# Optimization experiments

Measured on AMD Instinct MI355X. Metric: run time of the kernel, lower is better.

## Reference

```python
import jax, jax.numpy as jnp
import numpy as np

H, DK = 4, 64
D = H * DK              # hidden_dim = 256
D_OUT = 64
L = 2
NT, ET = 2, 3
AUTHOR, PAPER = 0, 1                 # sorted ntypes: ['author','paper']
CITES, WRITES, WRITTEN_BY = 0, 1, 2  # sorted etypes: ['cites','writes','written-by']
NA, NPAPER = 20000, 40000
E_WB, E_W, E_C = 150000, 150000, 300000
SQRT_DK = float(np.sqrt(DK))
EPS = 1e-5


def setup_inputs() -> dict:
    key = jax.random.key(0)
    ks = jax.random.split(key, 24)
    s = 1.0 / np.sqrt(D)
    return {
        "x_author": jax.random.normal(ks[0], (NA, D), jnp.float32),
        "x_paper": jax.random.normal(ks[1], (NPAPER, D), jnp.float32),
        "ew_wb": jax.random.uniform(ks[2], (E_WB,), jnp.float32),
        "ew_w": jax.random.uniform(ks[3], (E_W,), jnp.float32),
        "ew_c": jax.random.uniform(ks[4], (E_C,), jnp.float32),
        "adapt_W": jax.random.normal(ks[5], (NT, D, D), jnp.float32) * s,
        "adapt_b": jnp.zeros((NT, D), jnp.float32),
        "kW": jax.random.normal(ks[6], (L, NT, D, D), jnp.float32) * s,
        "kb": jnp.zeros((L, NT, D), jnp.float32),
        "qW": jax.random.normal(ks[7], (L, NT, D, D), jnp.float32) * s,
        "qb": jnp.zeros((L, NT, D), jnp.float32),
        "mW": jax.random.normal(ks[8], (L, NT, D, D), jnp.float32) * s,
        "mb": jnp.zeros((L, NT, D), jnp.float32),
        "aW": jax.random.normal(ks[9], (L, NT, D, D), jnp.float32) * s,
        "ab": jnp.zeros((L, NT, D), jnp.float32),
        "w_pri": jnp.ones((L, ET, H), jnp.float32),
        "w_att": jax.random.normal(ks[10], (L, ET, H, DK, DK), jnp.float32) / np.sqrt(DK),
        "w_msg": jax.random.normal(ks[11], (L, ET, H, DK, DK), jnp.float32) / np.sqrt(DK),
        "skip": jnp.ones((L, ET), jnp.float32),
        "ln_g": jnp.ones((L, NT, D), jnp.float32),
        "ln_b": jnp.zeros((L, NT, D), jnp.float32),
        "out_W": jax.random.normal(ks[12], (D, D_OUT), jnp.float32) * s,
        "out_b": jnp.zeros((D_OUT,), jnp.float32),
        "src_wb": jax.random.randint(ks[13], (E_WB,), 0, NPAPER, jnp.int32),
        "dst_wb": jax.random.randint(ks[14], (E_WB,), 0, NA, jnp.int32),
        "src_w": jax.random.randint(ks[15], (E_W,), 0, NA, jnp.int32),
        "dst_w": jax.random.randint(ks[16], (E_W,), 0, NPAPER, jnp.int32),
        "src_c": jax.random.randint(ks[17], (E_C,), 0, NPAPER, jnp.int32),
        "dst_c": jax.random.randint(ks[18], (E_C,), 0, NPAPER, jnp.int32),
    }


def _ln(x, g, b):
    mu = x.mean(-1, keepdims=True)
    var = ((x - mu) ** 2).mean(-1, keepdims=True)
    return (x - mu) * jax.lax.rsqrt(var + EPS) * g + b


def _hgt_layer(feats, rels, kW, kb, qW, qb, mW, mb, aW, ab,
               w_pri, w_att, w_msg, skip, ln_g, ln_b):
    # feats: [x_author, x_paper]; per-ntype K/Q/M projections -> [N, H, DK]
    Ns = [f.shape[0] for f in feats]
    kbase = [(feats[t] @ kW[t] + kb[t]).reshape(-1, H, DK) for t in range(NT)]
    qbase = [(feats[t] @ qW[t] + qb[t]).reshape(-1, H, DK) for t in range(NT)]
    mbase = [(feats[t] @ mW[t] + mb[t]).reshape(-1, H, DK) for t in range(NT)]
    aggs = {}
    for (st, e, dt, src, dst, ew) in rels:
        k = jnp.einsum('nhd,hde->nhe', kbase[st], w_att[e])
        m = jnp.einsum('nhd,hde->nhe', mbase[st], w_msg[e])
        score = (qbase[dt][dst] * k[src]).sum(-1) * w_pri[e] / SQRT_DK  # [E, H]
        attn = jax.nn.sigmoid(score) * ew[:, None]
        msg = m[src] * attn[:, :, None]                                 # [E, H, DK]
        aggs[e] = jax.ops.segment_sum(msg, dst, num_segments=Ns[dt])
    # cross_reducer='mean': mean over relation aggregates per dst ntype
    t_author = aggs[WRITTEN_BY].reshape(Ns[AUTHOR], D)
    t_paper = ((aggs[WRITES] + aggs[CITES]) * 0.5).reshape(Ns[PAPER], D)
    new = []
    for nid, t in ((AUTHOR, t_author), (PAPER, t_paper)):
        alpha = jax.nn.sigmoid(skip[nid])  # skip indexed by n_id (as in source)
        tr = t @ aW[nid] + ab[nid]
        o = tr * alpha + feats[nid] * (1.0 - alpha)
        new.append(_ln(o, ln_g[nid], ln_b[nid]))
    return new


def _forward(x_author, x_paper, ew_wb, ew_w, ew_c,
             adapt_W, adapt_b, kW, kb, qW, qb, mW, mb, aW, ab,
             w_pri, w_att, w_msg, skip, ln_g, ln_b, out_W, out_b,
             src_wb, dst_wb, src_w, dst_w, src_c, dst_c):
    feats = [
        jax.nn.gelu(x_author @ adapt_W[AUTHOR] + adapt_b[AUTHOR], approximate=False),
        jax.nn.gelu(x_paper @ adapt_W[PAPER] + adapt_b[PAPER], approximate=False),
    ]
    rels = [
        (PAPER, WRITTEN_BY, AUTHOR, src_wb, dst_wb, ew_wb),
        (AUTHOR, WRITES, PAPER, src_w, dst_w, ew_w),
        (PAPER, CITES, PAPER, src_c, dst_c, ew_c),
    ]
    for l in range(L):
        feats = _hgt_layer(feats, rels, kW[l], kb[l], qW[l], qb[l], mW[l], mb[l],
                           aW[l], ab[l], w_pri[l], w_att[l], w_msg[l], skip[l],
                           ln_g[l], ln_b[l])
    return feats[PAPER] @ out_W + out_b  # out_key = 'paper'


def reference(x_author, x_paper, ew_wb, ew_w, ew_c,
              adapt_W, adapt_b, kW, kb, qW, qb, mW, mb, aW, ab,
              w_pri, w_att, w_msg, skip, ln_g, ln_b, out_W, out_b,
              src_wb, dst_wb, src_w, dst_w, src_c, dst_c):
    return _forward(x_author, x_paper, ew_wb, ew_w, ew_c,
                    adapt_W, adapt_b, kW, kb, qW, qb, mW, mb, aW, ab,
                    w_pri, w_att, w_msg, skip, ln_g, ln_b, out_W, out_b,
                    src_wb, dst_wb, src_w, dst_w, src_c, dst_c)
```

## Files before the change

### kernel.cpp

```cpp
#include <hip/hip_runtime.h>
#include <hip/hip_bf16.h>
#include <math.h>

using bf16 = __hip_bfloat16;

typedef __attribute__((ext_vector_type(8))) short short8;
typedef __attribute__((ext_vector_type(4))) float float4v;

static constexpr int kNA  = 20000;
static constexpr int kNP  = 40000;
static constexpr int kEWB = 150000;
static constexpr int kEW  = 150000;
static constexpr int kEC  = 300000;

static constexpr int kNSeg = 21;
static constexpr int kSegN[kNSeg] = {
  150000, 150000, 300000,
  131072, 512,
  262144, 1024,
  262144, 1024,
  262144, 1024,
  262144, 1024,
  24,
  98304, 98304,
  6, 1024, 1024,
  16384, 64
};
static constexpr size_t kOff(int s) {
  size_t o = 0;
  for (int i = 0; i < s; ++i) o += (size_t)kSegN[i];
  return o;
}
static constexpr size_t kCanonTotal = kOff(kNSeg);

struct CanonArgs {
  const void* src[kNSeg];
  int n[kNSeg];
  unsigned dstOff[kNSeg];
};
struct TransArgs {
  const bf16* src[10];
  bf16* dst[10];
};
struct GemmDesc {
  const short* wt;
  const bf16* bias;
  void* c;
  int ldc;
  int coff;
  int act;
  int otype;
  int pad;
};
struct MultiDesc { GemmDesc d[6]; };
struct ScanArgs {
  int* deg[3];
  int* offs[3];
  int* bsums;
  int N[3];
};

__device__ __forceinline__ float toF(float x) { return x; }
__device__ __forceinline__ float toF(bf16 x)  { return __bfloat162float(x); }
__device__ __forceinline__ float bits2f(unsigned short b) {
  unsigned int u = ((unsigned int)b) << 16;
  return __uint_as_float(u);
}
__device__ __forceinline__ float sigmoidf_(float x) { return 1.0f / (1.0f + expf(-x)); }
__device__ __forceinline__ float gelu_exact(float x) {
  return 0.5f * x * (1.0f + erff(x * 0.70710678118654752f));
}

__global__ __launch_bounds__(256) void detect_dtype(
    const unsigned* __restrict__ x, unsigned* __restrict__ flags)
{
  __shared__ int cnt;
  if (threadIdx.x == 0) cnt = 0;
  __syncthreads();
  unsigned w = x[threadIdx.x];
  unsigned e = (w >> 7) & 0xFFu;
  if (e >= 110u && e <= 140u) atomicAdd(&cnt, 1);
  __syncthreads();
  if (threadIdx.x == 0) {
    flags[0] = (cnt >= 128) ? 1u : 0u;
    flags[1] = 1u;
  }
}

__global__ __launch_bounds__(256) void canon_kernel(
    CanonArgs a, bf16* __restrict__ dst, const unsigned* __restrict__ flags)
{
  const int s = blockIdx.y;
  const int i = blockIdx.x * 256 + threadIdx.x;
  if (i >= a.n[s]) return;
  bf16 v;
  if (flags[0]) v = ((const bf16*)a.src[s])[i];
  else          v = __float2bfloat16(((const float*)a.src[s])[i]);
  dst[a.dstOff[s] + i] = v;
}

__global__ __launch_bounds__(256) void transpose_w(TransArgs ta)
{
  const int m = blockIdx.z;
  const short* src = (const short*)ta.src[m];
  short* dst = (short*)ta.dst[m];
  const int k0 = blockIdx.x * 64, n0 = blockIdx.y * 64;
  __shared__ short tile[64][65];
  const int tx = threadIdx.x & 63, ty = threadIdx.x >> 6;
  for (int i = ty; i < 64; i += 4)
    tile[i][tx] = src[(size_t)(k0 + i) * 256 + n0 + tx];
  __syncthreads();
  for (int i = ty; i < 64; i += 4)
    dst[(size_t)(n0 + i) * 256 + k0 + tx] = tile[tx][i];
}

__global__ __launch_bounds__(256) void csr_hist(
    const int* __restrict__ dst, int E, int* __restrict__ cnt)
{
  const int i = blockIdx.x * 256 + threadIdx.x;
  if (i < E) atomicAdd(&cnt[dst[i]], 1);
}

__global__ __launch_bounds__(256) void scan_l1(ScanArgs a)
{
  const int rel = blockIdx.y;
  const int N = a.N[rel];
  const int t = threadIdx.x;
  const int lane = t & 63;
  const int wid = t >> 6;
  const int i0 = blockIdx.x * 2048 + t * 8;
  const int* deg = a.deg[rel];
  int v[8];
  int T = 0;
  #pragma unroll
  for (int j = 0; j < 8; ++j) {
    v[j] = (i0 + j < N) ? deg[i0 + j] : 0;
    T += v[j];
  }
  int incl = T;
  #pragma unroll
  for (int off = 1; off < 64; off <<= 1) {
    const int u = __shfl_up(incl, off);
    if (lane >= off) incl += u;
  }
  __shared__ int wsum[4];
  if (lane == 63) wsum[wid] = incl;
  __syncthreads();
  int woff = 0;
  #pragma unroll
  for (int wp = 0; wp < 4; ++wp) if (wp < wid) woff += wsum[wp];
  int run = woff + incl - T;
  int* offs = a.offs[rel];
  #pragma unroll
  for (int j = 0; j < 8; ++j) {
    if (i0 + j < N) offs[i0 + j] = run;
    run += v[j];
  }
  if (t == 0)
    a.bsums[rel * 32 + blockIdx.x] = wsum[0] + wsum[1] + wsum[2] + wsum[3];
}

__global__ __launch_bounds__(64) void scan_l2(int* __restrict__ bsums,
                                              int* __restrict__ totals)
{
  const int rel = blockIdx.x;
  const int lane = threadIdx.x;
  const int v = (lane < 32) ? bsums[rel * 32 + lane] : 0;
  int incl = v;
  #pragma unroll
  for (int off = 1; off < 64; off <<= 1) {
    const int u = __shfl_up(incl, off);
    if (lane >= off) incl += u;
  }
  if (lane < 32) bsums[rel * 32 + lane] = incl - v;
  if (lane == 63) totals[rel] = incl;
}

__global__ __launch_bounds__(256) void scan_l3(ScanArgs a,
                                               const int* __restrict__ totals)
{
  const int rel = blockIdx.y;
  const int N = a.N[rel];
  const int i0 = blockIdx.x * 2048 + threadIdx.x * 8;
  const int boff = a.bsums[rel * 32 + blockIdx.x];
  int* offs = a.offs[rel];
  int* cur = a.deg[rel];
  #pragma unroll
  for (int j = 0; j < 8; ++j) {
    const int idx = i0 + j;
    if (idx < N) {
      const int o = offs[idx] + boff;
      offs[idx] = o;
      cur[idx] = o;
    }
  }
  if (blockIdx.x == 0 && threadIdx.x == 0) offs[N] = totals[rel];
}

__global__ __launch_bounds__(256) void csr_scatter(
    const int* __restrict__ dst, const int* __restrict__ src,
    const bf16* __restrict__ ew, int E, int* __restrict__ cur,
    int* __restrict__ srcs, bf16* __restrict__ ews)
{
  const int i = blockIdx.x * 256 + threadIdx.x;
  if (i >= E) return;
  const int p = atomicAdd(&cur[dst[i]], 1);
  srcs[p] = src[i];
  ews[p]  = ew[i];
}

__global__ __launch_bounds__(256) void combine_weights(
    const bf16* __restrict__ Wbig, const bf16* __restrict__ bbig,
    const bf16* __restrict__ wsm, bf16* __restrict__ KMT,
    bf16* __restrict__ kmb, int noff)
{
  const int blk = blockIdx.y;
  const int rc  = blockIdx.x;
  const int h = blk & 3;
  const int le = blk >> 2;
  const int e = le % 3;
  const int l = le / 3;
  const int st = (e == 1) ? 0 : 1;

  const short* Wsrc = (const short*)(Wbig + (size_t)(l * 2 + st) * 65536);
  const bf16*  bsrc = bbig + (size_t)(l * 2 + st) * 256;
  const short* wm   = (const short*)(wsm + ((size_t)(l * 3 + e) * 4 + h) * 4096);
  short* outT = (short*)(KMT + (size_t)(l * 3 + e) * 512 * 256);
  bf16* outb  = kmb + (size_t)(l * 3 + e) * 512;

  __shared__ short w[64][72];
  __shared__ short As[32][72];
  __shared__ short ot[64][40];

  const int t = threadIdx.x;
  {
    const int base = t * 16;
    const int r0 = base >> 6, c0 = base & 63;
    *(short8*)&w[r0][c0]     = *(const short8*)&wm[base];
    *(short8*)&w[r0][c0 + 8] = *(const short8*)&wm[base + 8];
  }
  {
    const int row = t >> 3;
    const int kc = (t & 7) * 8;
    *(short8*)&As[row][kc] =
        *(const short8*)&Wsrc[(size_t)(rc * 32 + row) * 256 + h * 64 + kc];
  }
  __syncthreads();

  const int j   = t & 63;
  const int sub = t >> 6;
  float accv[8] = {};
  #pragma unroll
  for (int d = 0; d < 64; ++d) {
    const float wd = bits2f((unsigned short)w[d][j]);
    #pragma unroll
    for (int r8 = 0; r8 < 8; ++r8)
      accv[r8] += bits2f((unsigned short)As[sub * 8 + r8][d]) * wd;
  }
  #pragma unroll
  for (int r8 = 0; r8 < 8; ++r8) {
    union { bf16 h; short s; } cv;
    cv.h = __float2bfloat16(accv[r8]);
    ot[j][sub * 8 + r8] = cv.s;
  }

  if (rc == 0 && t < 64) {
    float acc = 0.f;
    #pragma unroll
    for (int d = 0; d < 64; ++d)
      acc += toF(bsrc[h * 64 + d]) * bits2f((unsigned short)w[d][t]);
    outb[h * 64 + t + noff] = __float2bfloat16(acc);
  }
  __syncthreads();
  {
    const int nn = t >> 2;
    const int kx = (t & 3) * 8;
    short8 v;
    #pragma unroll
    for (int x = 0; x < 8; ++x) v[x] = ot[nn][kx + x];
    *(short8*)&outT[(size_t)(h * 64 + nn + noff) * 256 + rc * 32 + kx] = v;
  }
}

__global__ __launch_bounds__(256, 4) void mfma_gemm128(
    const void* __restrict__ A, const unsigned* __restrict__ aflag,
    MultiDesc md, int M)
{
  __shared__ short As[128][72];
  __shared__ short Bs[128][72];
  const GemmDesc d = md.d[blockIdx.y];
  const bool abf = (*aflag != 0u);
  const int t = threadIdx.x;
  const int bm = blockIdx.x * 128;
  const int lane = t & 63;
  const int wid  = t >> 6;
  const int wm = (wid >> 1) * 64;
  const int wn = (wid & 1) * 64;
  const int col16 = lane & 15;
  const int quad  = lane >> 4;
  const int rr = t >> 3;
  const int kk = (t & 7) * 8;

  float4v acc[4][4];
  #pragma unroll
  for (int mi = 0; mi < 4; ++mi)
    #pragma unroll
    for (int ni = 0; ni < 4; ++ni) acc[mi][ni] = (float4v){0.f, 0.f, 0.f, 0.f};

  for (int k0 = 0; k0 < 256; k0 += 64) {
    #pragma unroll
    for (int it = 0; it < 4; ++it) {
      const int row = it * 32 + rr;
      const int grow = bm + row;
      short8 v = (short8){0, 0, 0, 0, 0, 0, 0, 0};
      if (grow < M) {
        if (abf) {
          v = *(const short8*)((const short*)A + (size_t)grow * 256 + k0 + kk);
        } else {
          const float* ap = (const float*)A + (size_t)grow * 256 + k0 + kk;
          #pragma unroll
          for (int j = 0; j < 8; ++j) {
            union { bf16 h; short s; } cv;
            cv.h = __float2bfloat16(ap[j]);
            v[j] = cv.s;
          }
        }
      }
      *(short8*)&As[row][kk] = v;
    }
    #pragma unroll
    for (int it = 0; it < 4; ++it) {
      const int n = it * 32 + rr;
      *(short8*)&Bs[n][kk] = *(const short8*)&d.wt[(size_t)n * 256 + k0 + kk];
    }
    __syncthreads();

    #pragma unroll
    for (int ks = 0; ks < 64; ks += 32) {
      short8 bfr[4];
      #pragma unroll
      for (int ni = 0; ni < 4; ++ni)
        bfr[ni] = *(const short8*)&Bs[wn + ni * 16 + col16][ks + quad * 8];
      #pragma unroll
      for (int mi = 0; mi < 4; ++mi) {
        const short8 afr = *(const short8*)&As[wm + mi * 16 + col16][ks + quad * 8];
        #pragma unroll
        for (int ni = 0; ni < 4; ++ni)
          acc[mi][ni] = __builtin_amdgcn_mfma_f32_16x16x32_bf16(afr, bfr[ni], acc[mi][ni], 0, 0, 0);
      }
    }
    __syncthreads();
  }

  #pragma unroll
  for (int ni = 0; ni < 4; ++ni) {
    const int col = wn + ni * 16 + col16;
    const float bc = toF(d.bias[col]);
    const int gcol = d.coff + col;
    #pragma unroll
    for (int mi = 0; mi < 4; ++mi) {
      #pragma unroll
      for (int r = 0; r < 4; ++r) {
        const int row = bm + wm + mi * 16 + quad * 4 + r;
        if (row < M) {
          float v = acc[mi][ni][r] + bc;
          if (d.act == 1) v = gelu_exact(v);
          const size_t idx = (size_t)row * d.ldc + gcol;
          if (d.otype == 0) ((bf16*)d.c)[idx] = __float2bfloat16(v);
          else              ((float*)d.c)[idx] = v;
        }
      }
    }
  }
}

__global__ __launch_bounds__(256) void gather_kernel(
    const bf16* __restrict__ q, const bf16* __restrict__ km,
    const int* __restrict__ srcs, const bf16* __restrict__ ews,
    const int* __restrict__ offs, const bf16* __restrict__ pri,
    bf16* __restrict__ agg, int Nd, int addPrev, float finalScale)
{
  const int lane = threadIdx.x & 63;
  const int wid  = threadIdx.x >> 6;
  const int node = blockIdx.x * 4 + wid;
  if (node >= Nd) return;
  const int h  = lane >> 5;
  const int sl = lane & 31;
  const float prih = toF(pri[sl >> 3]);

  union B8 { uint4 u; unsigned short s[8]; };
  B8 qv;
  qv.u = ((const uint4*)(q + (size_t)node * 256))[sl];
  float qf[8];
  #pragma unroll
  for (int j = 0; j < 8; ++j) qf[j] = bits2f(qv.s[j]);

  float acc[8] = {};
  const int beg = offs[node], end = offs[node + 1];
  for (int idx = beg + h; idx < end; idx += 2) {
    const int s = srcs[idx];
    const float w = toF(ews[idx]);
    B8 kb;
    kb.u = ((const uint4*)(km + (size_t)s * 512))[sl];
    float dot = 0.f;
    #pragma unroll
    for (int j = 0; j < 8; ++j) dot += qf[j] * bits2f(kb.s[j]);
    dot += __shfl_xor(dot, 1);
    dot += __shfl_xor(dot, 2);
    dot += __shfl_xor(dot, 4);
    const float a = w * sigmoidf_(dot * prih * 0.125f);
    B8 mb;
    mb.u = ((const uint4*)(km + (size_t)s * 512 + 256))[sl];
    #pragma unroll
    for (int j = 0; j < 8; ++j) acc[j] += bits2f(mb.s[j]) * a;
  }

  #pragma unroll
  for (int j = 0; j < 8; ++j) acc[j] += __shfl_xor(acc[j], 32);

  if (h == 0) {
    bf16* out = agg + (size_t)node * 256 + sl * 8;
    if (addPrev) {
      B8 pb;
      pb.u = *(const uint4*)out;
      #pragma unroll
      for (int j = 0; j < 8; ++j) acc[j] += bits2f(pb.s[j]);
    }
    B8 ov;
    #pragma unroll
    for (int j = 0; j < 8; ++j) {
      union { bf16 h; unsigned short u; } cv;
      cv.h = __float2bfloat16(acc[j] * finalScale);
      ov.s[j] = cv.u;
    }
    *(uint4*)out = ov.u;
  }
}

__global__ __launch_bounds__(256) void skip_ln(
    const float* __restrict__ tr, bf16* __restrict__ feat,
    const bf16* __restrict__ skipv, const bf16* __restrict__ g,
    const bf16* __restrict__ b, int N)
{
  const int lane = threadIdx.x & 63;
  const int wid  = threadIdx.x >> 6;
  const int node = blockIdx.x * 4 + wid;
  if (node >= N) return;
  const float alpha = sigmoidf_(toF(*skipv));
  const float4 t = ((const float4*)(tr + (size_t)node * 256))[lane];
  union B4 { uint2 u; unsigned short s[4]; };
  B4 fb;
  fb.u = ((const uint2*)(feat + (size_t)node * 256))[lane];
  float o[4];
  o[0] = t.x * alpha + bits2f(fb.s[0]) * (1.f - alpha);
  o[1] = t.y * alpha + bits2f(fb.s[1]) * (1.f - alpha);
  o[2] = t.z * alpha + bits2f(fb.s[2]) * (1.f - alpha);
  o[3] = t.w * alpha + bits2f(fb.s[3]) * (1.f - alpha);

  float sum = o[0] + o[1] + o[2] + o[3];
  #pragma unroll
  for (int off = 32; off; off >>= 1) sum += __shfl_xor(sum, off);
  const float mu = sum * (1.f / 256.f);

  float dd[4], sq = 0.f;
  #pragma unroll
  for (int j = 0; j < 4; ++j) { dd[j] = o[j] - mu; sq += dd[j] * dd[j]; }
  #pragma unroll
  for (int off = 32; off; off >>= 1) sq += __shfl_xor(sq, off);
  const float rs = rsqrtf(sq * (1.f / 256.f) + 1e-5f);

  bf16* fout = feat + (size_t)node * 256 + lane * 4;
  #pragma unroll
  for (int j = 0; j < 4; ++j) {
    float r = dd[j] * rs * toF(g[lane * 4 + j]) + toF(b[lane * 4 + j]);
    fout[j] = __float2bfloat16(r);
  }
}

__global__ __launch_bounds__(256) void out_gemm(
    const bf16* __restrict__ A, const bf16* __restrict__ W,
    const bf16* __restrict__ bias, void* __restrict__ out,
    const unsigned* __restrict__ flag, int M)
{
  __shared__ float Ws[64][64];
  const bool obf = (*flag != 0u);
  const int tid = threadIdx.x;
  const int row = blockIdx.x * 64 + (tid >> 2);
  const int c0 = (tid & 3) * 16;
  const int arow = (row < M) ? row : 0;
  const bf16* a = A + (size_t)arow * 256;
  float acc[16] = {};
  for (int k0 = 0; k0 < 256; k0 += 64) {
    for (int i = tid; i < 4096; i += 256)
      Ws[i >> 6][i & 63] = toF(W[(size_t)(k0 + (i >> 6)) * 64 + (i & 63)]);
    __syncthreads();
    for (int k = 0; k < 64; ++k) {
      const float av = toF(a[k0 + k]);
      #pragma unroll
      for (int j = 0; j < 16; ++j) acc[j] += av * Ws[k][c0 + j];
    }
    __syncthreads();
  }
  if (row < M) {
    #pragma unroll
    for (int j = 0; j < 16; ++j) {
      const float v = acc[j] + toF(bias[c0 + j]);
      const size_t idx = (size_t)row * 64 + c0 + j;
      if (obf) ((bf16*)out)[idx] = __float2bfloat16(v);
      else     ((float*)out)[idx] = v;
    }
  }
}

extern "C" void kernel_launch(void* const* d_in, const int* in_sizes, int n_in,
                              void* d_out, int out_size, void* d_ws, size_t ws_size,
                              hipStream_t stream) {
  const int* src_wb  = (const int*)d_in[23];
  const int* dst_wb  = (const int*)d_in[24];
  const int* src_w   = (const int*)d_in[25];
  const int* dst_w   = (const int*)d_in[26];
  const int* src_c   = (const int*)d_in[27];
  const int* dst_c   = (const int*)d_in[28];

  char* base = (char*)d_ws;
  unsigned* flags = (unsigned*)base;
  bf16* canon = (bf16*)(base + 256);
  char* p = base + 256 + (((size_t)kCanonTotal * 2 + 511) & ~(size_t)511);
  bf16* adWT = (bf16*)p;
  bf16* qWT  = adWT + (size_t)2 * 65536;
  bf16* aWT  = qWT  + (size_t)4 * 65536;
  bf16* KMeffT = aWT + (size_t)4 * 65536;
  bf16* kmbeT  = KMeffT + (size_t)6 * 512 * 256;
  char* pc = (char*)(((size_t)(kmbeT + 6 * 512) + 511) & ~(size_t)511);
  int* cur_wb  = (int*)pc;
  int* cur_w   = cur_wb + (kNA + 1);
  int* cur_c   = cur_w + (kNP + 1);
  int* offs_wb = cur_c + (kNP + 1);
  int* offs_w  = offs_wb + (kNA + 1);
  int* offs_c  = offs_w + (kNP + 1);
  int* srcs_wb = offs_c + (kNP + 1);
  int* srcs_w  = srcs_wb + kEWB;
  int* srcs_c  = srcs_w + kEW;
  bf16* ews_wb = (bf16*)(srcs_c + kEC);
  bf16* ews_w  = ews_wb + kEWB;
  bf16* ews_c  = ews_w + kEW;
  int* bsums   = (int*)(ews_c + kEC);
  int* totals  = bsums + 96;
  char* p2 = (char*)(((size_t)(totals + 3) + 511) & ~(size_t)511);
  bf16* fa  = (bf16*)p2;
  bf16* fp_ = fa + (size_t)kNA * 256;
  char* R   = (char*)(fp_ + (size_t)kNP * 256);
  bf16* qa   = (bf16*)R;
  bf16* qp   = qa + (size_t)kNA * 256;
  bf16* km_a = qp + (size_t)kNP * 256;
  bf16* km_p = km_a + (size_t)kNA * 512;
  float* tr_a = (float*)R;
  float* tr_p = tr_a + (size_t)kNA * 256;
  char* afterR = R + ((size_t)(kNA + kNP) * 256 + (size_t)(kNA + kNP) * 512) * sizeof(bf16);
  bf16* agg_a = (bf16*)afterR;
  bf16* agg_p = agg_a + (size_t)kNA * 256;

  const bf16* c_ew_wb = canon + kOff(0);
  const bf16* c_ew_w  = canon + kOff(1);
  const bf16* c_ew_c  = canon + kOff(2);
  const bf16* c_adW   = canon + kOff(3);
  const bf16* c_adb   = canon + kOff(4);
  const bf16* c_kW    = canon + kOff(5);
  const bf16* c_kb    = canon + kOff(6);
  const bf16* c_qW    = canon + kOff(7);
  const bf16* c_qb    = canon + kOff(8);
  const bf16* c_mW    = canon + kOff(9);
  const bf16* c_mb    = canon + kOff(10);
  const bf16* c_aW    = canon + kOff(11);
  const bf16* c_ab    = canon + kOff(12);
  const bf16* c_wpri  = canon + kOff(13);
  const bf16* c_watt  = canon + kOff(14);
  const bf16* c_wmsg  = canon + kOff(15);
  const bf16* c_skip  = canon + kOff(16);
  const bf16* c_lng   = canon + kOff(17);
  const bf16* c_lnb   = canon + kOff(18);
  const bf16* c_outW  = canon + kOff(19);
  const bf16* c_outb  = canon + kOff(20);

  const unsigned* fIn = flags + 0;
  const unsigned* f1  = flags + 1;

  detect_dtype<<<1, 256, 0, stream>>>((const unsigned*)d_in[0], flags);

  CanonArgs ca;
  for (int s = 0; s < kNSeg; ++s) { ca.n[s] = kSegN[s]; ca.dstOff[s] = (unsigned)kOff(s); }
  const int srcIdx[kNSeg] = {2,3,4, 5,6, 7,8, 9,10, 11,12, 13,14, 15, 16,17, 18,19,20, 21,22};
  for (int s = 0; s < kNSeg; ++s) ca.src[s] = d_in[srcIdx[s]];
  canon_kernel<<<dim3(1172, kNSeg), 256, 0, stream>>>(ca, canon, flags);

  TransArgs ta;
  ta.src[0] = c_adW;              ta.dst[0] = adWT;
  ta.src[1] = c_adW + 65536;      ta.dst[1] = adWT + 65536;
  for (int m = 0; m < 4; ++m) { ta.src[2 + m] = c_qW + (size_t)m * 65536; ta.dst[2 + m] = qWT + (size_t)m * 65536; }
  for (int m = 0; m < 4; ++m) { ta.src[6 + m] = c_aW + (size_t)m * 65536; ta.dst[6 + m] = aWT + (size_t)m * 65536; }
  transpose_w<<<dim3(4, 4, 10), 256, 0, stream>>>(ta);

  hipMemsetAsync(cur_wb, 0, (size_t)((kNA + 1) + 2 * (kNP + 1)) * 4, stream);
  csr_hist<<<(kEWB + 255) / 256, 256, 0, stream>>>(dst_wb, kEWB, cur_wb);
  csr_hist<<<(kEW  + 255) / 256, 256, 0, stream>>>(dst_w,  kEW,  cur_w);
  csr_hist<<<(kEC  + 255) / 256, 256, 0, stream>>>(dst_c,  kEC,  cur_c);
  ScanArgs sa;
  sa.deg[0] = cur_wb;  sa.offs[0] = offs_wb; sa.N[0] = kNA;
  sa.deg[1] = cur_w;   sa.offs[1] = offs_w;  sa.N[1] = kNP;
  sa.deg[2] = cur_c;   sa.offs[2] = offs_c;  sa.N[2] = kNP;
  sa.bsums = bsums;
  scan_l1<<<dim3(32, 3), 256, 0, stream>>>(sa);
  scan_l2<<<3, 64, 0, stream>>>(bsums, totals);
  scan_l3<<<dim3(20, 3), 256, 0, stream>>>(sa, totals);
  csr_scatter<<<(kEWB + 255) / 256, 256, 0, stream>>>(dst_wb, src_wb, c_ew_wb, kEWB, cur_wb, srcs_wb, ews_wb);
  csr_scatter<<<(kEW  + 255) / 256, 256, 0, stream>>>(dst_w,  src_w,  c_ew_w,  kEW,  cur_w,  srcs_w,  ews_w);
  csr_scatter<<<(kEC  + 255) / 256, 256, 0, stream>>>(dst_c,  src_c,  c_ew_c,  kEC,  cur_c,  srcs_c,  ews_c);

  combine_weights<<<dim3(8, 24), 256, 0, stream>>>(c_kW, c_kb, c_watt, KMeffT, kmbeT, 0);
  combine_weights<<<dim3(8, 24), 256, 0, stream>>>(c_mW, c_mb, c_wmsg, KMeffT, kmbeT, 256);

  auto grid = [](int m, int ny) { return dim3((unsigned)((m + 127) / 128), (unsigned)ny); };
  auto mkd = [](const bf16* wt, const bf16* bias, void* c, int ldc, int coff,
                int act, int otype) {
    GemmDesc g;
    g.wt = (const short*)wt; g.bias = bias; g.c = c; g.ldc = ldc;
    g.coff = coff; g.act = act; g.otype = otype; g.pad = 0;
    return g;
  };

  {
    MultiDesc md{};
    md.d[0] = mkd(adWT,                c_adb,        fa, 256, 0,   1, 0);
    md.d[1] = mkd(adWT + 128 * 256,    c_adb + 128,  fa, 256, 128, 1, 0);
    mfma_gemm128<<<grid(kNA, 2), 256, 0, stream>>>(d_in[0], fIn, md, kNA);
    md.d[0] = mkd(adWT + 65536,        c_adb + 256,  fp_, 256, 0,   1, 0);
    md.d[1] = mkd(adWT + 65536 + 128 * 256, c_adb + 384, fp_, 256, 128, 1, 0);
    mfma_gemm128<<<grid(kNP, 2), 256, 0, stream>>>(d_in[1], fIn, md, kNP);
  }

  for (int l = 0; l < 2; ++l) {
    const bf16* qW_a = qWT + (size_t)(l * 2 + 0) * 65536;
    const bf16* qW_p = qWT + (size_t)(l * 2 + 1) * 65536;
    const bf16* qb_a = c_qb + (l * 2 + 0) * 256;
    const bf16* qb_p = c_qb + (l * 2 + 1) * 256;
    const bf16* KM_c  = KMeffT + (size_t)(l * 3 + 0) * 512 * 256;
    const bf16* KM_w  = KMeffT + (size_t)(l * 3 + 1) * 512 * 256;
    const bf16* KM_wb = KMeffT + (size_t)(l * 3 + 2) * 512 * 256;
    const bf16* kb_c  = kmbeT + (l * 3 + 0) * 512;
    const bf16* kb_w  = kmbeT + (l * 3 + 1) * 512;
    const bf16* kb_wb = kmbeT + (l * 3 + 2) * 512;

    {
      MultiDesc md{};
      md.d[0] = mkd(qW_a,             qb_a,        qa,   256, 0,   0, 0);
      md.d[1] = mkd(qW_a + 128 * 256, qb_a + 128,  qa,   256, 128, 0, 0);
      for (int s = 0; s < 4; ++s)
        md.d[2 + s] = mkd(KM_w + (size_t)s * 128 * 256, kb_w + s * 128, km_a, 512, s * 128, 0, 0);
      mfma_gemm128<<<grid(kNA, 6), 256, 0, stream>>>(fa, f1, md, kNA);
    }
    {
      MultiDesc md{};
      md.d[0] = mkd(qW_p,             qb_p,        qp,   256, 0,   0, 0);
      md.d[1] = mkd(qW_p + 128 * 256, qb_p + 128,  qp,   256, 128, 0, 0);
      for (int s = 0; s < 4; ++s)
        md.d[2 + s] = mkd(KM_wb + (size_t)s * 128 * 256, kb_wb + s * 128, km_p, 512, s * 128, 0, 0);
      mfma_gemm128<<<grid(kNP, 6), 256, 0, stream>>>(fp_, f1, md, kNP);
    }

    gather_kernel<<<(kNA + 3) / 4, 256, 0, stream>>>(
        qa, km_p, srcs_wb, ews_wb, offs_wb, c_wpri + (l * 3 + 2) * 4,
        agg_a, kNA, 0, 1.f);
    gather_kernel<<<(kNP + 3) / 4, 256, 0, stream>>>(
        qp, km_a, srcs_w, ews_w, offs_w, c_wpri + (l * 3 + 1) * 4,
        agg_p, kNP, 0, 1.f);

    {
      MultiDesc md{};
      for (int s = 0; s < 4; ++s)
        md.d[s] = mkd(KM_c + (size_t)s * 128 * 256, kb_c + s * 128, km_p, 512, s * 128, 0, 0);
      mfma_gemm128<<<grid(kNP, 4), 256, 0, stream>>>(fp_, f1, md, kNP);
    }
    gather_kernel<<<(kNP + 3) / 4, 256, 0, stream>>>(
        qp, km_p, srcs_c, ews_c, offs_c, c_wpri + (l * 3 + 0) * 4,
        agg_p, kNP, 1, 0.5f);

    {
      const bf16* aW_a = aWT + (size_t)(l * 2 + 0) * 65536;
      const bf16* aW_p = aWT + (size_t)(l * 2 + 1) * 65536;
      MultiDesc md{};
      md.d[0] = mkd(aW_a,             c_ab + (l * 2 + 0) * 256,       tr_a, 256, 0,   0, 1);
      md.d[1] = mkd(aW_a + 128 * 256, c_ab + (l * 2 + 0) * 256 + 128, tr_a, 256, 128, 0, 1);
      mfma_gemm128<<<grid(kNA, 2), 256, 0, stream>>>(agg_a, f1, md, kNA);
      md.d[0] = mkd(aW_p,             c_ab + (l * 2 + 1) * 256,       tr_p, 256, 0,   0, 1);
      md.d[1] = mkd(aW_p + 128 * 256, c_ab + (l * 2 + 1) * 256 + 128, tr_p, 256, 128, 0, 1);
      mfma_gemm128<<<grid(kNP, 2), 256, 0, stream>>>(agg_p, f1, md, kNP);
    }

    skip_ln<<<kNA / 4, 256, 0, stream>>>(
        tr_a, fa,  c_skip + l * 3 + 0, c_lng + (l * 2 + 0) * 256, c_lnb + (l * 2 + 0) * 256, kNA);
    skip_ln<<<kNP / 4, 256, 0, stream>>>(
        tr_p, fp_, c_skip + l * 3 + 1, c_lng + (l * 2 + 1) * 256, c_lnb + (l * 2 + 1) * 256, kNP);
  }

  out_gemm<<<kNP / 64, 256, 0, stream>>>(fp_, c_outW, c_outb, d_out, fIn, kNP);
}
```

Before: 912.0 us.

## Fuse output GEMM with skip-mix and LayerNorm; group GEMM block order

Adds a GEMM kernel that computes the full 256-wide output tile per block, then applies the sigmoid skip blend, bias and LayerNorm in the epilogue with an in-block row reduction. This removes the fp32 tr_a/tr_p intermediate and the separate skip_ln launches. The generic GEMM also moves to a 1D grid that groups 8 M-tiles across all N-slabs so neighbouring blocks share A rows in cache. The fused kernel uses more registers and LDS (occupancy 2) and computes variance as E[x^2]-mu^2, which can lose some precision.

```diff
diff --git a/kernel.cpp b/kernel.cpp
--- a/kernel.cpp
+++ b/kernel.cpp
@@ -284,14 +284,20 @@
 
 __global__ __launch_bounds__(256, 4) void mfma_gemm128(
     const void* __restrict__ A, const unsigned* __restrict__ aflag,
-    MultiDesc md, int M)
+    MultiDesc md, int M, int ntiles, int nslab)
 {
   __shared__ short As[128][72];
   __shared__ short Bs[128][72];
-  const GemmDesc d = md.d[blockIdx.y];
+  const int lid = blockIdx.x;
+  const int grp = lid / (8 * nslab);
+  const int rem = lid - grp * 8 * nslab;
+  const int slab = rem >> 3;
+  const int tx = grp * 8 + (rem & 7);
+  if (tx >= ntiles) return;
+  const GemmDesc d = md.d[slab];
   const bool abf = (*aflag != 0u);
   const int t = threadIdx.x;
-  const int bm = blockIdx.x * 128;
+  const int bm = tx * 128;
   const int lane = t & 63;
   const int wid  = t >> 6;
   const int wm = (wid >> 1) * 64;
@@ -374,6 +380,146 @@
   }
 }
 
+__global__ __launch_bounds__(256, 2) void mfma_gemm_ln(
+    const bf16* __restrict__ A, const short* __restrict__ WT,
+    const bf16* __restrict__ bias, bf16* __restrict__ feat,
+    const bf16* __restrict__ skipv, const bf16* __restrict__ g,
+    const bf16* __restrict__ bvec, int M)
+{
+  __shared__ short As[128][72];
+  __shared__ short Bs[256][72];
+  __shared__ float redS[4][64];
+  __shared__ float redQ[4][64];
+  const int t = threadIdx.x;
+  const int bm = blockIdx.x * 128;
+  const int lane = t & 63;
+  const int wid  = t >> 6;
+  const int wm = (wid >> 1) * 64;
+  const int wn = (wid & 1) * 64;
+  const int col16 = lane & 15;
+  const int quad  = lane >> 4;
+  const int rr = t >> 3;
+  const int kk = (t & 7) * 8;
+
+  float4v acc[2][4][4];
+  #pragma unroll
+  for (int s = 0; s < 2; ++s)
+    #pragma unroll
+    for (int mi = 0; mi < 4; ++mi)
+      #pragma unroll
+      for (int ni = 0; ni < 4; ++ni) acc[s][mi][ni] = (float4v){0.f, 0.f, 0.f, 0.f};
+
+  for (int k0 = 0; k0 < 256; k0 += 64) {
+    #pragma unroll
+    for (int it = 0; it < 4; ++it) {
+      const int row = it * 32 + rr;
+      const int grow = bm + row;
+      short8 v = (short8){0, 0, 0, 0, 0, 0, 0, 0};
+      if (grow < M)
+        v = *(const short8*)((const short*)A + (size_t)grow * 256 + k0 + kk);
+      *(short8*)&As[row][kk] = v;
+    }
+    #pragma unroll
+    for (int it = 0; it < 8; ++it) {
+      const int n = it * 32 + rr;
+      *(short8*)&Bs[n][kk] = *(const short8*)&WT[(size_t)n * 256 + k0 + kk];
+    }
+    __syncthreads();
+
+    #pragma unroll
+    for (int ks = 0; ks < 64; ks += 32) {
+      short8 bfr[2][4];
+      #pragma unroll
+      for (int s = 0; s < 2; ++s)
+        #pragma unroll
+        for (int ni = 0; ni < 4; ++ni)
+          bfr[s][ni] = *(const short8*)&Bs[s * 128 + wn + ni * 16 + col16][ks + quad * 8];
+      #pragma unroll
+      for (int mi = 0; mi < 4; ++mi) {
+        const short8 afr = *(const short8*)&As[wm + mi * 16 + col16][ks + quad * 8];
+        #pragma unroll
+        for (int s = 0; s < 2; ++s)
+          #pragma unroll
+          for (int ni = 0; ni < 4; ++ni)
+            acc[s][mi][ni] = __builtin_amdgcn_mfma_f32_16x16x32_bf16(afr, bfr[s][ni], acc[s][mi][ni], 0, 0, 0);
+      }
+    }
+    __syncthreads();
+  }
+
+  const float alpha = sigmoidf_(toF(*skipv));
+  const float beta = 1.f - alpha;
+  float ps[4][4] = {};
+  float pq[4][4] = {};
+  #pragma unroll
+  for (int s = 0; s < 2; ++s) {
+    #pragma unroll
+    for (int ni = 0; ni < 4; ++ni) {
+      const int col = wn + s * 128 + ni * 16 + col16;
+      const float bc = toF(bias[col]);
+      #pragma unroll
+      for (int mi = 0; mi < 4; ++mi) {
+        #pragma unroll
+        for (int rg = 0; rg < 4; ++rg) {
+          const int row = bm + wm + mi * 16 + quad * 4 + rg;
+          float f = 0.f;
+          if (row < M) f = toF(feat[(size_t)row * 256 + col]);
+          const float o = (acc[s][mi][ni][rg] + bc) * alpha + f * beta;
+          acc[s][mi][ni][rg] = o;
+          ps[mi][rg] += o;
+          pq[mi][rg] += o * o;
+        }
+      }
+    }
+  }
+  #pragma unroll
+  for (int mi = 0; mi < 4; ++mi)
+    #pragma unroll
+    for (int rg = 0; rg < 4; ++rg) {
+      #pragma unroll
+      for (int off = 1; off < 16; off <<= 1) {
+        ps[mi][rg] += __shfl_xor(ps[mi][rg], off);
+        pq[mi][rg] += __shfl_xor(pq[mi][rg], off);
+      }
+    }
+  if (col16 == 0) {
+    #pragma unroll
+    for (int mi = 0; mi < 4; ++mi)
+      #pragma unroll
+      for (int rg = 0; rg < 4; ++rg) {
+        const int rl = mi * 16 + quad * 4 + rg;
+        redS[wid][rl] = ps[mi][rg];
+        redQ[wid][rl] = pq[mi][rg];
+      }
+  }
+  __syncthreads();
+  const int pbase = (wid >> 1) * 2;
+  #pragma unroll
+  for (int mi = 0; mi < 4; ++mi) {
+    #pragma unroll
+    for (int rg = 0; rg < 4; ++rg) {
+      const int rl = mi * 16 + quad * 4 + rg;
+      const float s1 = redS[pbase][rl] + redS[pbase + 1][rl];
+      const float s2 = redQ[pbase][rl] + redQ[pbase + 1][rl];
+      const float mu = s1 * (1.f / 256.f);
+      float var = s2 * (1.f / 256.f) - mu * mu;
+      var = fmaxf(var, 0.f);
+      const float rs = rsqrtf(var + 1e-5f);
+      const int row = bm + wm + mi * 16 + quad * 4 + rg;
+      if (row < M) {
+        #pragma unroll
+        for (int s = 0; s < 2; ++s)
+          #pragma unroll
+          for (int ni = 0; ni < 4; ++ni) {
+            const int col = wn + s * 128 + ni * 16 + col16;
+            const float r = (acc[s][mi][ni][rg] - mu) * rs * toF(g[col]) + toF(bvec[col]);
+            feat[(size_t)row * 256 + col] = __float2bfloat16(r);
+          }
+      }
+    }
+  }
+}
+
 __global__ __launch_bounds__(256) void gather_kernel(
     const bf16* __restrict__ q, const bf16* __restrict__ km,
     const int* __restrict__ srcs, const bf16* __restrict__ ews,
@@ -434,46 +580,6 @@
       ov.s[j] = cv.u;
     }
     *(uint4*)out = ov.u;
-  }
-}
-
-__global__ __launch_bounds__(256) void skip_ln(
-    const float* __restrict__ tr, bf16* __restrict__ feat,
-    const bf16* __restrict__ skipv, const bf16* __restrict__ g,
-    const bf16* __restrict__ b, int N)
-{
-  const int lane = threadIdx.x & 63;
-  const int wid  = threadIdx.x >> 6;
-  const int node = blockIdx.x * 4 + wid;
-  if (node >= N) return;
-  const float alpha = sigmoidf_(toF(*skipv));
-  const float4 t = ((const float4*)(tr + (size_t)node * 256))[lane];
-  union B4 { uint2 u; unsigned short s[4]; };
-  B4 fb;
-  fb.u = ((const uint2*)(feat + (size_t)node * 256))[lane];
-  float o[4];
-  o[0] = t.x * alpha + bits2f(fb.s[0]) * (1.f - alpha);
-  o[1] = t.y * alpha + bits2f(fb.s[1]) * (1.f - alpha);
-  o[2] = t.z * alpha + bits2f(fb.s[2]) * (1.f - alpha);
-  o[3] = t.w * alpha + bits2f(fb.s[3]) * (1.f - alpha);
-
-  float sum = o[0] + o[1] + o[2] + o[3];
-  #pragma unroll
-  for (int off = 32; off; off >>= 1) sum += __shfl_xor(sum, off);
-  const float mu = sum * (1.f / 256.f);
-
-  float dd[4], sq = 0.f;
-  #pragma unroll
-  for (int j = 0; j < 4; ++j) { dd[j] = o[j] - mu; sq += dd[j] * dd[j]; }
-  #pragma unroll
-  for (int off = 32; off; off >>= 1) sq += __shfl_xor(sq, off);
-  const float rs = rsqrtf(sq * (1.f / 256.f) + 1e-5f);
-
-  bf16* fout = feat + (size_t)node * 256 + lane * 4;
-  #pragma unroll
-  for (int j = 0; j < 4; ++j) {
-    float r = dd[j] * rs * toF(g[lane * 4 + j]) + toF(b[lane * 4 + j]);
-    fout[j] = __float2bfloat16(r);
   }
 }
 
@@ -554,8 +660,6 @@
   bf16* qp   = qa + (size_t)kNA * 256;
   bf16* km_a = qp + (size_t)kNP * 256;
   bf16* km_p = km_a + (size_t)kNA * 512;
-  float* tr_a = (float*)R;
-  float* tr_p = tr_a + (size_t)kNA * 256;
   char* afterR = R + ((size_t)(kNA + kNP) * 256 + (size_t)(kNA + kNP) * 512) * sizeof(bf16);
   bf16* agg_a = (bf16*)afterR;
   bf16* agg_p = agg_a + (size_t)kNA * 256;
@@ -619,7 +723,11 @@
   combine_weights<<<dim3(8, 24), 256, 0, stream>>>(c_kW, c_kb, c_watt, KMeffT, kmbeT, 0);
   combine_weights<<<dim3(8, 24), 256, 0, stream>>>(c_mW, c_mb, c_wmsg, KMeffT, kmbeT, 256);
 
-  auto grid = [](int m, int ny) { return dim3((unsigned)((m + 127) / 128), (unsigned)ny); };
+  auto sgrid = [](int m, int nslab) {
+    const int nt = (m + 127) / 128;
+    return dim3((unsigned)(((nt + 7) / 8) * 8 * nslab));
+  };
+  auto ntl = [](int m) { return (m + 127) / 128; };
   auto mkd = [](const bf16* wt, const bf16* bias, void* c, int ldc, int coff,
                 int act, int otype) {
     GemmDesc g;
@@ -632,10 +740,10 @@
     MultiDesc md{};
     md.d[0] = mkd(adWT,                c_adb,        fa, 256, 0,   1, 0);
     md.d[1] = mkd(adWT + 128 * 256,    c_adb + 128,  fa, 256, 128, 1, 0);
-    mfma_gemm128<<<grid(kNA, 2), 256, 0, stream>>>(d_in[0], fIn, md, kNA);
+    mfma_gemm128<<<sgrid(kNA, 2), 256, 0, stream>>>(d_in[0], fIn, md, kNA, ntl(kNA), 2);
     md.d[0] = mkd(adWT + 65536,        c_adb + 256,  fp_, 256, 0,   1, 0);
     md.d[1] = mkd(adWT + 65536 + 128 * 256, c_adb + 384, fp_, 256, 128, 1, 0);
-    mfma_gemm128<<<grid(kNP, 2), 256, 0, stream>>>(d_in[1], fIn, md, kNP);
+    mfma_gemm128<<<sgrid(kNP, 2), 256, 0, stream>>>(d_in[1], fIn, md, kNP, ntl(kNP), 2);
   }
 
   for (int l = 0; l < 2; ++l) {
@@ -656,7 +764,7 @@
       md.d[1] = mkd(qW_a + 128 * 256, qb_a + 128,  qa,   256, 128, 0, 0);
       for (int s = 0; s < 4; ++s)
         md.d[2 + s] = mkd(KM_w + (size_t)s * 128 * 256, kb_w + s * 128, km_a, 512, s * 128, 0, 0);
-      mfma_gemm128<<<grid(kNA, 6), 256, 0, stream>>>(fa, f1, md, kNA);
+      mfma_gemm128<<<sgrid(kNA, 6), 256, 0, stream>>>(fa, f1, md, kNA, ntl(kNA), 6);
     }
     {
       MultiDesc md{};
@@ -664,7 +772,7 @@
       md.d[1] = mkd(qW_p + 128 * 256, qb_p + 128,  qp,   256, 128, 0, 0);
       for (int s = 0; s < 4; ++s)
         md.d[2 + s] = mkd(KM_wb + (size_t)s * 128 * 256, kb_wb + s * 128, km_p, 512, s * 128, 0, 0);
-      mfma_gemm128<<<grid(kNP, 6), 256, 0, stream>>>(fp_, f1, md, kNP);
+      mfma_gemm128<<<sgrid(kNP, 6), 256, 0, stream>>>(fp_, f1, md, kNP, ntl(kNP), 6);
     }
 
     gather_kernel<<<(kNA + 3) / 4, 256, 0, stream>>>(
@@ -678,28 +786,20 @@
       MultiDesc md{};
       for (int s = 0; s < 4; ++s)
         md.d[s] = mkd(KM_c + (size_t)s * 128 * 256, kb_c + s * 128, km_p, 512, s * 128, 0, 0);
-      mfma_gemm128<<<grid(kNP, 4), 256, 0, stream>>>(fp_, f1, md, kNP);
+      mfma_gemm128<<<sgrid(kNP, 4), 256, 0, stream>>>(fp_, f1, md, kNP, ntl(kNP), 4);
     }
     gather_kernel<<<(kNP + 3) / 4, 256, 0, stream>>>(
         qp, km_p, srcs_c, ews_c, offs_c, c_wpri + (l * 3 + 0) * 4,
         agg_p, kNP, 1, 0.5f);
 
-    {
-      const bf16* aW_a = aWT + (size_t)(l * 2 + 0) * 65536;
-      const bf16* aW_p = aWT + (size_t)(l * 2 + 1) * 65536;
-      MultiDesc md{};
-      md.d[0] = mkd(aW_a,             c_ab + (l * 2 + 0) * 256,       tr_a, 256, 0,   0, 1);
-      md.d[1] = mkd(aW_a + 128 * 256, c_ab + (l * 2 + 0) * 256 + 128, tr_a, 256, 128, 0, 1);
-      mfma_gemm128<<<grid(kNA, 2), 256, 0, stream>>>(agg_a, f1, md, kNA);
-      md.d[0] = mkd(aW_p,             c_ab + (l * 2 + 1) * 256,       tr_p, 256, 0,   0, 1);
-      md.d[1] = mkd(aW_p + 128 * 256, c_ab + (l * 2 + 1) * 256 + 128, tr_p, 256, 128, 0, 1);
-      mfma_gemm128<<<grid(kNP, 2), 256, 0, stream>>>(agg_p, f1, md, kNP);
-    }
-
-    skip_ln<<<kNA / 4, 256, 0, stream>>>(
-        tr_a, fa,  c_skip + l * 3 + 0, c_lng + (l * 2 + 0) * 256, c_lnb + (l * 2 + 0) * 256, kNA);
-    skip_ln<<<kNP / 4, 256, 0, stream>>>(
-        tr_p, fp_, c_skip + l * 3 + 1, c_lng + (l * 2 + 1) * 256, c_lnb + (l * 2 + 1) * 256, kNP);
+    mfma_gemm_ln<<<ntl(kNA), 256, 0, stream>>>(
+        agg_a, (const short*)(aWT + (size_t)(l * 2 + 0) * 65536),
+        c_ab + (l * 2 + 0) * 256, fa, c_skip + l * 3 + 0,
+        c_lng + (l * 2 + 0) * 256, c_lnb + (l * 2 + 0) * 256, kNA);
+    mfma_gemm_ln<<<ntl(kNP), 256, 0, stream>>>(
+        agg_p, (const short*)(aWT + (size_t)(l * 2 + 1) * 65536),
+        c_ab + (l * 2 + 1) * 256, fp_, c_skip + l * 3 + 1,
+        c_lng + (l * 2 + 1) * 256, c_lnb + (l * 2 + 1) * 256, kNP);
   }
 
   out_gemm<<<kNP / 64, 256, 0, stream>>>(fp_, c_outW, c_outb, d_out, fIn, kNP);
```

After: 1.041 ms. +14.2%, slower.
